# Kernel tuning notes

Measured on AMD Instinct MI355X. Metric: run time of the kernel, lower is better.

Reference implementation:

```python
import jax, jax.numpy as jnp
import numpy as np

D = 1024   # embd_dim
H = 4      # number of SelectiveAttentionModule heads (each full-dim)
B, S = 4, 2048


def _layernorm(x, g, b, eps=1e-5):
    mu = jnp.mean(x, axis=-1, keepdims=True)
    var = jnp.var(x, axis=-1, keepdims=True)
    return (x - mu) * jax.lax.rsqrt(var + eps) * g + b


def setup_inputs() -> dict:
    key = jax.random.key(0)
    ks = jax.random.split(key, 16)
    sd = 1.0 / np.sqrt(D)
    x = jax.random.normal(ks[0], (B, S, D), dtype=jnp.float32)
    # per-head Q/K/V projections, stacked over head dim H ([H, in, out] layout)
    Wq = jax.random.uniform(ks[1], (H, D, D), jnp.float32, -sd, sd)
    bq = jax.random.uniform(ks[2], (H, D), jnp.float32, -sd, sd)
    Wk = jax.random.uniform(ks[3], (H, D, D), jnp.float32, -sd, sd)
    bk = jax.random.uniform(ks[4], (H, D), jnp.float32, -sd, sd)
    Wv = jax.random.uniform(ks[5], (H, D, D), jnp.float32, -sd, sd)
    bv = jax.random.uniform(ks[6], (H, D), jnp.float32, -sd, sd)
    sd1 = 1.0 / np.sqrt(H * D)
    W1 = jax.random.uniform(ks[7], (H * D, D), jnp.float32, -sd1, sd1)  # [in, out]
    b1 = jax.random.uniform(ks[8], (D,), jnp.float32, -sd1, sd1)
    W2 = jax.random.uniform(ks[9], (D, D), jnp.float32, -sd, sd)
    b2 = jax.random.uniform(ks[10], (D,), jnp.float32, -sd, sd)
    g1 = jnp.ones((D,), jnp.float32)
    be1 = jnp.zeros((D,), jnp.float32)
    g2 = jnp.ones((D,), jnp.float32)
    be2 = jnp.zeros((D,), jnp.float32)
    return {"embedding_matrix": x, "Wq": Wq, "bq": bq, "Wk": Wk, "bk": bk,
            "Wv": Wv, "bv": bv, "W1": W1, "b1": b1, "g1": g1, "be1": be1,
            "W2": W2, "b2": b2, "g2": g2, "be2": be2}


def reference(embedding_matrix, Wq, bq, Wk, bk, Wv, bv, W1, b1, g1, be1, W2, b2, g2, be2):
    x = embedding_matrix  # [B, S, D]
    # batched per-head projections: [H, B, S, D]
    q = jnp.einsum('bsd,hde->hbse', x, Wq) + bq[:, None, None, :]
    k = jnp.einsum('bsd,hde->hbse', x, Wk) + bk[:, None, None, :]
    v = jnp.einsum('bsd,hde->hbse', x, Wv) + bv[:, None, None, :]
    scale = 1.0 / jnp.sqrt(jnp.asarray(D, x.dtype))
    scores = jnp.einsum('hbse,hbte->hbst', q, k) * scale  # [H, B, S, S]
    attn = jax.nn.softmax(scores, axis=-1)
    heads = jnp.einsum('hbst,hbte->hbse', attn, v)        # [H, B, S, D]
    # torch.cat([V1..V4], dim=-1) == heads reordered to [B, S, H*D]
    concat = jnp.moveaxis(heads, 0, 2).reshape(x.shape[0], x.shape[1], H * D)
    proj = concat @ W1 + b1                               # [B, S, D]
    y = _layernorm(x + proj, g1, be1)
    return _layernorm(y + (y @ W2 + b2), g2, be2)
```

## Files before the change

### kernel.cpp

```cpp
#include <hip/hip_runtime.h>

using u16 = unsigned short;
using u32 = unsigned int;
typedef __attribute__((ext_vector_type(8))) short s16x8;
typedef __attribute__((ext_vector_type(4))) float f32x4;

typedef uint4   __attribute__((may_alias)) uint4a;
typedef ushort4 __attribute__((may_alias)) ushort4a;
typedef float4  __attribute__((may_alias)) float4a;
typedef u16     __attribute__((may_alias)) u16a;
typedef s16x8   __attribute__((may_alias)) s16x8a;

#define D_ 1024
#define H_ 4
#define B_ 4
#define S_ 2048
#define M_ 8192

#define BM 128
#define BN 128
#define BK 32

__device__ __forceinline__ float bf2f(u16 u) { return __uint_as_float(((u32)u) << 16); }
__device__ __forceinline__ u16 f2bf(float f) {
  u32 b = __float_as_uint(f);
  return (u16)((b + 0x7fffu + ((b >> 16) & 1u)) >> 16);
}

__device__ __forceinline__ void gload_lds16(const u16* g, u16* l) {
  __builtin_amdgcn_global_load_lds(
      (const __attribute__((address_space(1))) void*)g,
      (__attribute__((address_space(3))) void*)l, 16, 0, 0);
}

__device__ __forceinline__ void swz_decomp(int& x, int& y, int& z) {
  const int gx = gridDim.x, gy = gridDim.y;
  const int nwg = gx * gy * gridDim.z;
  const int flat = (blockIdx.z * gy + blockIdx.y) * gx + blockIdx.x;
  const int swz = (flat & 7) * (nwg >> 3) + (flat >> 3);
  const int t = swz >> 4, i = swz & 15;
  const int tiles_X = (gx * gridDim.z) >> 2;
  const int X = (t % tiles_X) * 4 + (i & 3);
  y = (t / tiles_X) * 4 + (i >> 2);
  z = X / gx;
  x = X % gx;
}

__global__ __launch_bounds__(256) void cvt_f32_bf16(const float* __restrict__ in,
                                                    u16* __restrict__ out, long n4) {
  long stride = (long)gridDim.x * blockDim.x;
  for (long i = (long)blockIdx.x * blockDim.x + threadIdx.x; i < n4; i += stride) {
    float4 v = ((const float4a*)in)[i];
    ushort4 o;
    o.x = f2bf(v.x); o.y = f2bf(v.y); o.z = f2bf(v.z); o.w = f2bf(v.w);
    ((ushort4a*)out)[i] = o;
  }
}

__global__ __launch_bounds__(256) void tcvt(const float* __restrict__ in,
                                            u16* __restrict__ out, int K, int N,
                                            long s_in, long s_out) {
  __shared__ float t[32][33];
  const int z = blockIdx.z;
  in += (long)z * s_in;
  out += (long)z * s_out;
  const int n0 = blockIdx.x * 32, k0 = blockIdx.y * 32;
  const int tx = threadIdx.x & 31, ty = threadIdx.x >> 5;
#pragma unroll
  for (int i = 0; i < 32; i += 8) t[ty + i][tx] = in[(long)(k0 + ty + i) * N + n0 + tx];
  __syncthreads();
#pragma unroll
  for (int i = 0; i < 32; i += 8)
    out[(long)(n0 + ty + i) * K + k0 + tx] = f2bf(t[tx][ty + i]);
}

__global__ __launch_bounds__(256) void biascat(const float* __restrict__ bq,
                                               const float* __restrict__ bk,
                                               const float* __restrict__ bv,
                                               float* __restrict__ o) {
  int i = blockIdx.x * 256 + threadIdx.x;
  float v = (i < 4096) ? bq[i] : ((i < 8192) ? bk[i - 4096] : bv[i - 8192]);
  o[i] = v;
}

__global__ __launch_bounds__(256) void dred(const float* __restrict__ dpart,
                                            float* __restrict__ drow) {
  int t = blockIdx.x * 256 + threadIdx.x;
  int z = t >> 11, row = t & 2047;
  float s = 0.f;
#pragma unroll
  for (int p = 0; p < 32; ++p) s += dpart[((long)z * 32 + p) * 2048 + row];
  drow[t] = s;
}

__device__ __forceinline__ int lds_slot(int row, int ks) {
  return row * 4 + (ks ^ ((row >> 1) & 3));
}

template <int OUT_MODE, int HAS_BIAS, int ACC>
__global__ __launch_bounds__(256, 4) void gemm_bt(
    const u16* __restrict__ A, const u16* __restrict__ Bm, void* __restrict__ Cp,
    const float* __restrict__ bias, float* __restrict__ drow,
    int K, int lda, int ldb, int ldc,
    long sA, long sB, long sC, long sBias, float scale) {
  __shared__ u16 Al[2][BM * BK];
  __shared__ u16 Bl[2][BN * BK];
  int bx, by, z;
  swz_decomp(bx, by, z);
  A += (long)z * sA;
  Bm += (long)z * sB;
  const long coff = (long)z * sC;
  const int bm = by * BM, bn = bx * BN;
  const int tid = threadIdx.x;
  const int lane = tid & 63;
  const int w = tid >> 6;
  const int wr = w >> 1, wc = w & 1;
  f32x4 acc[4][4] = {};

  auto stage = [&](u16* Ad, u16* Bd, int k0) {
#pragma unroll
    for (int it = 0; it < 2; ++it) {
      const int sbase = w * 128 + it * 64;
      const int slot = sbase + lane;
      const int row = slot >> 2;
      const int j = (slot & 3) ^ ((row >> 1) & 3);
      gload_lds16(A + (long)(bm + row) * lda + (k0 + j * 8), Ad + sbase * 8);
      gload_lds16(Bm + (long)(bn + row) * ldb + (k0 + j * 8), Bd + sbase * 8);
    }
  };

  stage(Al[0], Bl[0], 0);
  __syncthreads();
  int cur = 0;
  for (int k0 = 0; k0 < K; k0 += BK) {
    const int nxt = cur ^ 1;
    if (k0 + BK < K) stage(Al[nxt], Bl[nxt], k0 + BK);
    const int ks = lane >> 4;
    s16x8 a[4], b[4];
#pragma unroll
    for (int i = 0; i < 4; i++) {
      int row = wr * 64 + i * 16 + (lane & 15);
      a[i] = *(const s16x8a*)&Al[cur][lds_slot(row, ks) * 8];
    }
#pragma unroll
    for (int j = 0; j < 4; j++) {
      int row = wc * 64 + j * 16 + (lane & 15);
      b[j] = *(const s16x8a*)&Bl[cur][lds_slot(row, ks) * 8];
    }
#pragma unroll
    for (int i = 0; i < 4; i++)
#pragma unroll
      for (int j = 0; j < 4; j++)
        acc[i][j] = __builtin_amdgcn_mfma_f32_16x16x32_bf16(a[i], b[j], acc[i][j], 0, 0, 0);
    __syncthreads();
    cur = nxt;
  }

  if (OUT_MODE == 4) {
#pragma unroll
    for (int i = 0; i < 4; i++) {
      int mbase = bm + wr * 64 + i * 16 + ((lane >> 4) << 2);
#pragma unroll
      for (int r = 0; r < 4; r++) {
        const int mm = mbase + r;
        float rowsum = 0.f;
#pragma unroll
        for (int j = 0; j < 4; j++) {
          int n = bn + wc * 64 + j * 16 + (lane & 15);
          float e = __expf(acc[i][j][r] * scale);
          ((u16a*)Cp)[coff + (long)mm * ldc + n] = f2bf(e);
          rowsum += e;
        }
        rowsum += __shfl_xor(rowsum, 1, 64);
        rowsum += __shfl_xor(rowsum, 2, 64);
        rowsum += __shfl_xor(rowsum, 4, 64);
        rowsum += __shfl_xor(rowsum, 8, 64);
        if ((lane & 15) == 0)
          drow[((long)z * 32 + (bx * 2 + wc)) * S_ + mm] = rowsum;
      }
    }
    return;
  }
  if (OUT_MODE == 5) {
#pragma unroll
    for (int i = 0; i < 4; i++) {
      int mbase = bm + wr * 64 + i * 16 + ((lane >> 4) << 2);
      float inv[4];
#pragma unroll
      for (int r = 0; r < 4; r++) inv[r] = 1.0f / drow[(long)z * S_ + mbase + r];
#pragma unroll
      for (int j = 0; j < 4; j++) {
        int n = bn + wc * 64 + j * 16 + (lane & 15);
#pragma unroll
        for (int r = 0; r < 4; r++) {
          ((u16a*)Cp)[coff + (long)(mbase + r) * ldc + n] = f2bf(acc[i][j][r] * inv[r]);
        }
      }
    }
    return;
  }
  const bool tpose = (OUT_MODE == 3 && z == 2);
#pragma unroll
  for (int i = 0; i < 4; i++) {
    int mbase = bm + wr * 64 + i * 16 + ((lane >> 4) << 2);
#pragma unroll
    for (int j = 0; j < 4; j++) {
      int n = bn + wc * 64 + j * 16 + (lane & 15);
      float bv = 0.f;
      if (HAS_BIAS) bv = bias[z * sBias + n];
      if (tpose) {
        ushort4 o;
        o.x = f2bf(acc[i][j][0] * scale + bv);
        o.y = f2bf(acc[i][j][1] * scale + bv);
        o.z = f2bf(acc[i][j][2] * scale + bv);
        o.w = f2bf(acc[i][j][3] * scale + bv);
        long idx = coff + (long)(mbase >> 11) * ((long)D_ * S_) + (long)n * S_ + (mbase & 2047);
        *(ushort4a*)&((u16a*)Cp)[idx] = o;
      } else {
#pragma unroll
        for (int r = 0; r < 4; r++) {
          float v = acc[i][j][r] * scale + bv;
          long idx = coff + (long)(mbase + r) * ldc + n;
          if (OUT_MODE == 1 || OUT_MODE == 3) {
            ((u16a*)Cp)[idx] = f2bf(v);
          } else {
            float* Cf = (float*)Cp;
            Cf[idx] = ACC ? (Cf[idx] + v) : v;
          }
        }
      }
    }
  }
}

__global__ __launch_bounds__(256) void ln_kernel(
    const float* __restrict__ X, const float* __restrict__ R,
    const float* __restrict__ g, const float* __restrict__ be,
    float* __restrict__ Y, u16* __restrict__ Yb) {
  const long row = blockIdx.x;
  const int t = threadIdx.x, lane = t & 63, w = t >> 6;
  const long base = row * 1024 + t * 4;
  float4 a = *(const float4a*)(X + base);
  float4 b = *(const float4a*)(R + base);
  float v0 = a.x + b.x, v1 = a.y + b.y, v2 = a.z + b.z, v3 = a.w + b.w;
  float s = v0 + v1 + v2 + v3;
  float q = v0 * v0 + v1 * v1 + v2 * v2 + v3 * v3;
#pragma unroll
  for (int o = 32; o > 0; o >>= 1) { s += __shfl_xor(s, o, 64); q += __shfl_xor(q, o, 64); }
  __shared__ float rs[4], rq[4];
  if (lane == 0) { rs[w] = s; rq[w] = q; }
  __syncthreads();
  s = rs[0] + rs[1] + rs[2] + rs[3];
  q = rq[0] + rq[1] + rq[2] + rq[3];
  const float mu = s * (1.f / 1024.f);
  const float var = q * (1.f / 1024.f) - mu * mu;
  const float rstd = rsqrtf(var + 1e-5f);
  float4 gv = *(const float4a*)(g + t * 4);
  float4 bv = *(const float4a*)(be + t * 4);
  float o0 = (v0 - mu) * rstd * gv.x + bv.x;
  float o1 = (v1 - mu) * rstd * gv.y + bv.y;
  float o2 = (v2 - mu) * rstd * gv.z + bv.z;
  float o3 = (v3 - mu) * rstd * gv.w + bv.w;
  float4 o4; o4.x = o0; o4.y = o1; o4.z = o2; o4.w = o3;
  *(float4a*)(Y + base) = o4;
  if (Yb) {
    ushort4 ob; ob.x = f2bf(o0); ob.y = f2bf(o1); ob.z = f2bf(o2); ob.w = f2bf(o3);
    *(ushort4a*)(Yb + base) = ob;
  }
}

extern "C" void kernel_launch(void* const* d_in, const int* in_sizes, int n_in,
                              void* d_out, int out_size, void* d_ws, size_t ws_size,
                              hipStream_t stream) {
  const float* x   = (const float*)d_in[0];
  const float* Wq  = (const float*)d_in[1];
  const float* bq  = (const float*)d_in[2];
  const float* Wk  = (const float*)d_in[3];
  const float* bk  = (const float*)d_in[4];
  const float* Wv  = (const float*)d_in[5];
  const float* bv  = (const float*)d_in[6];
  const float* W1  = (const float*)d_in[7];
  const float* b1  = (const float*)d_in[8];
  const float* g1  = (const float*)d_in[9];
  const float* be1 = (const float*)d_in[10];
  const float* W2  = (const float*)d_in[11];
  const float* b2  = (const float*)d_in[12];
  const float* g2  = (const float*)d_in[13];
  const float* be2 = (const float*)d_in[14];
  float* out = (float*)d_out;

  const size_t NEED_BASE = 186646528ULL;
  const size_t NEED_CC   = 203423744ULL;
  if (ws_size < NEED_BASE) return;
  const bool useCc = (ws_size >= NEED_CC);
  char* ws = (char*)d_ws;
  u16* xb  = (u16*)(ws + 0L);
  u16* Wqt = (u16*)(ws + 16777216L);
  u16* Wkt = (u16*)(ws + 25165824L);
  u16* Wvt = (u16*)(ws + 33554432L);
  u16* W1t = (u16*)(ws + 41943040L);
  u16* W2t = (u16*)(ws + 50331648L);
  u16* Qh  = (u16*)(ws + 52428800L);
  u16* Kh  = (u16*)(ws + 69206016L);
  u16* Vt  = (u16*)(ws + 85983232L);
  u16* Sbh = (u16*)(ws + 102760448L);
  u16* Cc   = (u16*)(ws + 136314880L);
  u16* Ch   = (u16*)(ws + 136314880L);
  float* proj = useCc ? (float*)Sbh : (float*)(ws + 153092096L);
  float* y  = (float*)Qh;
  u16*   yb = Vt;
  float* z2 = useCc ? (float*)Cc : proj;
  float* biasQKV = out;
  float* dsum  = out + 16384;
  float* dpart = out + 65536;

  dim3 blk(256);
  {
    long n4 = (long)M_ * D_ / 4;
    hipLaunchKernelGGL(cvt_f32_bf16, dim3(4096), blk, 0, stream, x, xb, n4);
  }
  hipLaunchKernelGGL(tcvt, dim3(32, 32, H_), blk, 0, stream, Wq, Wqt, D_, D_,
                     (long)D_ * D_, (long)D_ * D_);
  hipLaunchKernelGGL(tcvt, dim3(32, 32, H_), blk, 0, stream, Wk, Wkt, D_, D_,
                     (long)D_ * D_, (long)D_ * D_);
  hipLaunchKernelGGL(tcvt, dim3(32, 32, H_), blk, 0, stream, Wv, Wvt, D_, D_,
                     (long)D_ * D_, (long)D_ * D_);
  hipLaunchKernelGGL(tcvt, dim3(32, 128, 1), blk, 0, stream, W1, W1t, H_ * D_, D_, 0L, 0L);
  hipLaunchKernelGGL(tcvt, dim3(32, 32, 1), blk, 0, stream, W2, W2t, D_, D_, 0L, 0L);
  hipLaunchKernelGGL(biascat, dim3(48), blk, 0, stream, bq, bk, bv, biasQKV);

  for (int h = 0; h < H_; ++h) {
    const long wo = (long)h * D_ * D_;
    hipLaunchKernelGGL((gemm_bt<3, 1, 0>), dim3(8, 64, 3), blk, 0, stream,
                       xb, Wqt + wo, (void*)Qh, biasQKV + (long)h * D_, (float*)nullptr,
                       D_, D_, D_, D_,
                       0L, (long)H_ * D_ * D_, (long)M_ * D_, (long)H_ * D_, 1.0f);
    hipLaunchKernelGGL((gemm_bt<4, 0, 0>), dim3(16, 16, B_), blk, 0, stream,
                       Qh, Kh, (void*)Sbh, (const float*)nullptr, dpart,
                       D_, D_, D_, S_,
                       (long)S_ * D_, (long)S_ * D_, (long)S_ * S_, 0L, 0.03125f);
    hipLaunchKernelGGL(dred, dim3(32), blk, 0, stream, dpart, dsum);
    if (useCc) {
      hipLaunchKernelGGL((gemm_bt<5, 0, 0>), dim3(8, 16, B_), blk, 0, stream,
                         Sbh, Vt, (void*)(Cc + (long)h * D_), (const float*)nullptr, dsum,
                         S_, S_, S_, H_ * D_,
                         (long)S_ * S_, (long)D_ * S_, (long)S_ * H_ * D_, 0L, 1.0f);
    } else {
      hipLaunchKernelGGL((gemm_bt<5, 0, 0>), dim3(8, 16, B_), blk, 0, stream,
                         Sbh, Vt, (void*)Ch, (const float*)nullptr, dsum,
                         S_, S_, S_, D_,
                         (long)S_ * S_, (long)D_ * S_, (long)S_ * D_, 0L, 1.0f);
      if (h == 0) {
        hipLaunchKernelGGL((gemm_bt<0, 1, 0>), dim3(8, 64, 1), blk, 0, stream,
                           Ch, W1t + (long)h * D_, (void*)proj, b1, (float*)nullptr,
                           D_, D_, H_ * D_, D_, 0L, 0L, 0L, 0L, 1.0f);
      } else {
        hipLaunchKernelGGL((gemm_bt<0, 0, 1>), dim3(8, 64, 1), blk, 0, stream,
                           Ch, W1t + (long)h * D_, (void*)proj, (const float*)nullptr,
                           (float*)nullptr, D_, D_, H_ * D_, D_, 0L, 0L, 0L, 0L, 1.0f);
      }
    }
  }

  if (useCc) {
    hipLaunchKernelGGL((gemm_bt<0, 1, 0>), dim3(8, 64, 1), blk, 0, stream,
                       Cc, W1t, (void*)proj, b1, (float*)nullptr,
                       H_ * D_, H_ * D_, H_ * D_, D_, 0L, 0L, 0L, 0L, 1.0f);
  }

  hipLaunchKernelGGL(ln_kernel, dim3(M_), blk, 0, stream, x, proj, g1, be1, y, yb);

  hipLaunchKernelGGL((gemm_bt<0, 1, 0>), dim3(8, 64, 1), blk, 0, stream,
                     yb, W2t, (void*)z2, b2, (float*)nullptr,
                     D_, D_, D_, D_, 0L, 0L, 0L, 0L, 1.0f);

  hipLaunchKernelGGL(ln_kernel, dim3(M_), blk, 0, stream, y, z2, g2, be2, out, (u16*)nullptr);
}
```

Measured before the change: 858.8 us.

## Replace QK^T score GEMM with 256x256-tile 8-wave pipelined kernel

Adds a dedicated 512-thread kernel for the Q·K^T score GEMM that computes 256x256 output tiles with BK=64, XOR-swizzled LDS, direct global-to-LDS loads and a hand-scheduled double-buffer interleaving quarter-tile MFMA batches with staged loads under explicit barriers and vmcnt waits. The exp and partial row-sum epilogue moves into this kernel, and the old OUT_MODE 4 path is removed. The larger tile raises arithmetic intensity and the explicit schedule aims to overlap loads with MFMA. The cost is fewer workgroups (256 per head), more LDS and registers per block, and a fragile hand-written wait/barrier scheme.

```diff
diff --git a/kernel.cpp b/kernel.cpp
--- a/kernel.cpp
+++ b/kernel.cpp
@@ -32,6 +32,10 @@
       (const __attribute__((address_space(1))) void*)g,
       (__attribute__((address_space(3))) void*)l, 16, 0, 0);
 }
+
+#define FENCE asm volatile("" ::: "memory")
+#define BAR do { FENCE; __builtin_amdgcn_s_barrier(); FENCE; } while (0)
+#define VMC4 asm volatile("s_waitcnt vmcnt(4)" ::: "memory")
 
 __device__ __forceinline__ void swz_decomp(int& x, int& y, int& z) {
   const int gx = gridDim.x, gy = gridDim.y;
@@ -91,6 +95,151 @@
 #pragma unroll
   for (int p = 0; p < 32; ++p) s += dpart[((long)z * 32 + p) * 2048 + row];
   drow[t] = s;
+}
+
+__device__ __forceinline__ s16x8 lds_frag(const u16* buf, int r, int jc) {
+  return *(const s16x8a*)&buf[(((r << 3) + (jc ^ (r & 7)))) << 3];
+}
+__device__ __forceinline__ void readB(const u16* Bbuf, int wc, int lane, s16x8 (&bfr)[4][2]) {
+#pragma unroll
+  for (int j = 0; j < 4; ++j)
+#pragma unroll
+    for (int s = 0; s < 2; ++s)
+      bfr[j][s] = lds_frag(Bbuf, wc * 64 + j * 16 + (lane & 15), 4 * s + (lane >> 4));
+}
+__device__ __forceinline__ void readA(const u16* Abuf, int q, int wr, int lane, s16x8 (&afr)[2][2]) {
+#pragma unroll
+  for (int il = 0; il < 2; ++il)
+#pragma unroll
+    for (int s = 0; s < 2; ++s)
+      afr[il][s] = lds_frag(Abuf, wr * 128 + (q * 2 + il) * 16 + (lane & 15), 4 * s + (lane >> 4));
+}
+__device__ __forceinline__ void mfma_quad(const s16x8 (&afr)[2][2], const s16x8 (&bfr)[4][2],
+                                          f32x4 (&acc)[8][4], int q) {
+  __builtin_amdgcn_s_setprio(1);
+#pragma unroll
+  for (int s = 0; s < 2; ++s)
+#pragma unroll
+    for (int il = 0; il < 2; ++il)
+#pragma unroll
+      for (int j = 0; j < 4; ++j)
+        acc[q * 2 + il][j] =
+            __builtin_amdgcn_mfma_f32_16x16x32_bf16(afr[il][s], bfr[j][s], acc[q * 2 + il][j], 0, 0, 0);
+  __builtin_amdgcn_s_setprio(0);
+}
+
+__global__ __launch_bounds__(512, 2) void gemm256x(
+    const u16* __restrict__ A, const u16* __restrict__ Bm, u16* __restrict__ Cp,
+    float* __restrict__ dpart) {
+  __shared__ u16 Al[2][16384];
+  __shared__ u16 Bl[2][16384];
+  const int flat = (blockIdx.z * 8 + blockIdx.y) * 8 + blockIdx.x;
+  const int swz = (flat & 7) * 32 + (flat >> 3);
+  const int bx = swz & 7, by = (swz >> 3) & 7, z = swz >> 6;
+  A += (long)z * ((long)S_ * D_);
+  Bm += (long)z * ((long)S_ * D_);
+  const long coff = (long)z * S_ * S_;
+  const int bm = by * 256, bn = bx * 256;
+  const int tid = threadIdx.x;
+  const int lane = tid & 63;
+  const int w = tid >> 6;
+  const int wr = w >> 2, wc = w & 3;
+  f32x4 acc[8][4] = {};
+  const int nt2 = D_ >> 7;
+
+  auto stage = [&](const u16* src, int b0, u16* lbuf, int h, int kt) {
+    const int k0 = kt << 6;
+#pragma unroll
+    for (int it = 0; it < 2; ++it) {
+      int c = w * 128 + it * 64 + lane;
+      int row = h * 128 + (c >> 3);
+      int j = (c & 7) ^ (row & 7);
+      gload_lds16(src + (long)(b0 + row) * D_ + (k0 + j * 8),
+                  lbuf + ((h * 1024 + w * 128 + it * 64) << 3));
+    }
+  };
+
+  stage(A, bm, Al[0], 0, 0);
+  stage(A, bm, Al[0], 1, 0);
+  stage(Bm, bn, Bl[0], 0, 0);
+  stage(Bm, bn, Bl[0], 1, 0);
+  stage(Bm, bn, Bl[1], 0, 1);
+  stage(Bm, bn, Bl[1], 1, 1);
+  VMC4;
+  BAR;
+
+  s16x8 bfr[4][2];
+  for (int i2 = 0; i2 < nt2; ++i2) {
+    const int t = i2 * 2;
+    s16x8 afr[2][2];
+    readB(Bl[0], wc, lane, bfr);
+    readA(Al[0], 0, wr, lane, afr);
+    stage(A, bm, Al[1], 0, t + 1);
+    BAR;
+    mfma_quad(afr, bfr, acc, 0);
+    BAR;
+    readA(Al[0], 1, wr, lane, afr);
+    stage(A, bm, Al[1], 1, t + 1);
+    BAR;
+    mfma_quad(afr, bfr, acc, 1);
+    BAR;
+    readA(Al[0], 2, wr, lane, afr);
+    stage(Bm, bn, Bl[0], 0, t + 2);
+    BAR;
+    mfma_quad(afr, bfr, acc, 2);
+    BAR;
+    readA(Al[0], 3, wr, lane, afr);
+    stage(Bm, bn, Bl[0], 1, t + 2);
+    BAR;
+    mfma_quad(afr, bfr, acc, 3);
+    VMC4;
+    BAR;
+    readB(Bl[1], wc, lane, bfr);
+    readA(Al[1], 0, wr, lane, afr);
+    stage(A, bm, Al[0], 0, t + 2);
+    BAR;
+    mfma_quad(afr, bfr, acc, 0);
+    BAR;
+    readA(Al[1], 1, wr, lane, afr);
+    stage(A, bm, Al[0], 1, t + 2);
+    BAR;
+    mfma_quad(afr, bfr, acc, 1);
+    BAR;
+    readA(Al[1], 2, wr, lane, afr);
+    stage(Bm, bn, Bl[1], 0, t + 3);
+    BAR;
+    mfma_quad(afr, bfr, acc, 2);
+    BAR;
+    readA(Al[1], 3, wr, lane, afr);
+    stage(Bm, bn, Bl[1], 1, t + 3);
+    BAR;
+    mfma_quad(afr, bfr, acc, 3);
+    VMC4;
+    BAR;
+  }
+
+#pragma unroll
+  for (int i = 0; i < 8; i++) {
+    int mbase = bm + wr * 128 + i * 16 + ((lane >> 4) << 2);
+#pragma unroll
+    for (int r = 0; r < 4; r++) {
+      const int mm = mbase + r;
+      float rowsum = 0.f;
+#pragma unroll
+      for (int j = 0; j < 4; j++) {
+        int n = bn + wc * 64 + j * 16 + (lane & 15);
+        float e = __expf(acc[i][j][r] * 0.03125f);
+        ((u16a*)Cp)[coff + (long)mm * S_ + n] = f2bf(e);
+        rowsum += e;
+      }
+      rowsum += __shfl_xor(rowsum, 1, 64);
+      rowsum += __shfl_xor(rowsum, 2, 64);
+      rowsum += __shfl_xor(rowsum, 4, 64);
+      rowsum += __shfl_xor(rowsum, 8, 64);
+      if ((lane & 15) == 0)
+        dpart[((long)z * 32 + (bx * 4 + wc)) * S_ + mm] = rowsum;
+    }
+  }
 }
 
 __device__ __forceinline__ int lds_slot(int row, int ks) {
@@ -156,31 +305,6 @@
     cur = nxt;
   }
 
-  if (OUT_MODE == 4) {
-#pragma unroll
-    for (int i = 0; i < 4; i++) {
-      int mbase = bm + wr * 64 + i * 16 + ((lane >> 4) << 2);
-#pragma unroll
-      for (int r = 0; r < 4; r++) {
-        const int mm = mbase + r;
-        float rowsum = 0.f;
-#pragma unroll
-        for (int j = 0; j < 4; j++) {
-          int n = bn + wc * 64 + j * 16 + (lane & 15);
-          float e = __expf(acc[i][j][r] * scale);
-          ((u16a*)Cp)[coff + (long)mm * ldc + n] = f2bf(e);
-          rowsum += e;
-        }
-        rowsum += __shfl_xor(rowsum, 1, 64);
-        rowsum += __shfl_xor(rowsum, 2, 64);
-        rowsum += __shfl_xor(rowsum, 4, 64);
-        rowsum += __shfl_xor(rowsum, 8, 64);
-        if ((lane & 15) == 0)
-          drow[((long)z * 32 + (bx * 2 + wc)) * S_ + mm] = rowsum;
-      }
-    }
-    return;
-  }
   if (OUT_MODE == 5) {
 #pragma unroll
     for (int i = 0; i < 4; i++) {
@@ -335,10 +459,8 @@
                        xb, Wqt + wo, (void*)Qh, biasQKV + (long)h * D_, (float*)nullptr,
                        D_, D_, D_, D_,
                        0L, (long)H_ * D_ * D_, (long)M_ * D_, (long)H_ * D_, 1.0f);
-    hipLaunchKernelGGL((gemm_bt<4, 0, 0>), dim3(16, 16, B_), blk, 0, stream,
-                       Qh, Kh, (void*)Sbh, (const float*)nullptr, dpart,
-                       D_, D_, D_, S_,
-                       (long)S_ * D_, (long)S_ * D_, (long)S_ * S_, 0L, 0.03125f);
+    hipLaunchKernelGGL(gemm256x, dim3(8, 8, B_), dim3(512), 0, stream,
+                       Qh, Kh, Sbh, dpart);
     hipLaunchKernelGGL(dred, dim3(32), blk, 0, stream, dpart, dsum);
     if (useCc) {
       hipLaunchKernelGGL((gemm_bt<5, 0, 0>), dim3(8, 16, B_), blk, 0, stream,
```

New measurement: 821.1 us. 1.05x faster.
